# Optimization experiments

Hardware: AMD Instinct MI355X
Metric: run time of the kernel (lower is better)

## Reference

```python
import jax, jax.numpy as jnp
import numpy as np

BATCH, T, N = 8, 2048, 512


def setup_inputs() -> dict:
    key = jax.random.key(0)
    ks = jax.random.split(key, 8)
    scale = 1.0 / np.sqrt(2.0 * (N + N) / 2.0) / np.sqrt(2.0)  # GlorotNormal / sqrt(2)
    u = jax.random.normal(ks[0], (BATCH, T, N), dtype=jnp.float32)
    C_re = jax.random.normal(ks[1], (N, N), dtype=jnp.float32) * scale
    C_im = jax.random.normal(ks[2], (N, N), dtype=jnp.float32) * scale
    B_re = jax.random.normal(ks[3], (N, N), dtype=jnp.float32) * scale
    B_im = jax.random.normal(ks[4], (N, N), dtype=jnp.float32) * scale
    D = jax.random.normal(ks[5], (N,), dtype=jnp.float32)
    # nu drawn from the numerically-stable end of [log(-log rmax), log(-log rmin)]
    nu = jax.random.uniform(ks[6], (N,), minval=-4.6, maxval=-3.7, dtype=jnp.float32)
    theta = jax.random.uniform(ks[7], (N,), minval=0.0, maxval=3.14 / 10, dtype=jnp.float32)
    # gamma initialized as sqrt(1 - |lambda|^2), lambda = exp(-exp(nu) + i*theta)
    gamma = jnp.sqrt(1.0 - jnp.exp(-2.0 * jnp.exp(nu)))
    return {"u": u, "C_re": C_re, "C_im": C_im, "B_re": B_re, "B_im": B_im,
            "D": D, "nu": nu, "theta": theta, "gamma": gamma}


def reference(u, C_re, C_im, B_re, B_im, D, nu, theta, gamma):
    # log_lambda = -exp(nu) + i*theta  (the TF code names this `lambda_`)
    log_lam = (-jnp.exp(nu)).astype(jnp.complex64) + 1j * theta.astype(jnp.complex64)  # (n,)
    t = jnp.arange(u.shape[1], dtype=jnp.float32).astype(jnp.complex64)[:, None]       # (T,1)
    lam_pow = jnp.exp(log_lam[None, :] * t)    # (T,n) == diag(Lambda^t)
    lam_minpow = jnp.exp(-log_lam[None, :] * t)  # (T,n) == diag(Lambda^-t)
    Bm = (B_re + 1j * B_im).astype(jnp.complex64)  # (n,n)
    Cm = (C_re + 1j * C_im).astype(jnp.complex64)  # (n,n)
    # new_u = (gamma * u) @ B   (complex)
    new_u = (gamma * u).astype(jnp.complex64) @ Bm  # (b,t,n)
    # diag einsums in the original are elementwise multiplies
    x = jnp.cumsum(new_u * lam_minpow[None], axis=1) * lam_pow[None]  # (b,t,n)
    y = jnp.real(x @ Cm) + D * u
    return y
```

## Files before the change

### kernel.cpp

```cpp
#include <hip/hip_runtime.h>
#include <hip/hip_bf16.h>
#include <math.h>
#include <stdint.h>

#define BATCH 8
#define T_LEN 2048
#define NDIM 512
#define M_ROWS (BATCH * T_LEN)
#define CHUNK 32
#define NCHUNK (T_LEN / CHUNK)

typedef __attribute__((ext_vector_type(8))) short bf16x8;
typedef __attribute__((ext_vector_type(4))) float floatx4;

__device__ __forceinline__ unsigned short f2bf(float f) {
    union { float f; unsigned u; } v; v.f = f;
    unsigned r = v.u + 0x7fff + ((v.u >> 16) & 1);
    return (unsigned short)(r >> 16);
}
__device__ __forceinline__ float bf2f(unsigned short h) {
    union { unsigned u; float f; } v; v.u = ((unsigned)h) << 16;
    return v.f;
}
__device__ __forceinline__ float bf2f_lo(unsigned u) {
    union { unsigned u; float f; } v; v.u = u << 16; return v.f;
}
__device__ __forceinline__ float bf2f_hi(unsigned u) {
    union { unsigned u; float f; } v; v.u = u & 0xffff0000u; return v.f;
}

__device__ __forceinline__ void gld_lds16(const unsigned short* g, unsigned short* l) {
    __builtin_amdgcn_global_load_lds(
        (const __attribute__((address_space(1))) unsigned int*)(uintptr_t)g,
        (__attribute__((address_space(3))) unsigned int*)(uintptr_t)l,
        16, 0, 0);
}

__global__ __launch_bounds__(256) void k_prep(
    const float* __restrict__ u,
    const float* __restrict__ Bre, const float* __restrict__ Bim,
    const float* __restrict__ Cre, const float* __restrict__ Cim,
    const float* __restrict__ gamma,
    unsigned short* __restrict__ ubf,
    unsigned short* __restrict__ BT, unsigned short* __restrict__ CT)
{
    __shared__ unsigned short tile[32][33];
    const int blk = blockIdx.x;
    if (blk < 4096) {
        size_t i = ((size_t)blk * 256 + threadIdx.x) * 8;
        float4 a = *(const float4*)&u[i];
        float4 b = *(const float4*)&u[i + 4];
        ushort4 p0, p1;
        p0.x = f2bf(a.x); p0.y = f2bf(a.y); p0.z = f2bf(a.z); p0.w = f2bf(a.w);
        p1.x = f2bf(b.x); p1.y = f2bf(b.y); p1.z = f2bf(b.z); p1.w = f2bf(b.w);
        *(ushort4*)&ubf[i] = p0;
        *(ushort4*)&ubf[i + 4] = p1;
        return;
    }
    const int p = blk - 4096;
    const int z = p >> 8;
    const int rem = p & 255;
    const int n0 = (rem & 15) * 32, k0 = (rem >> 4) * 32;
    const float* __restrict__ src = (z == 0) ? Bre : (z == 1) ? Bim : (z == 2) ? Cre : Cim;
    const int tx = threadIdx.x & 31, ty = threadIdx.x >> 5;

#pragma unroll
    for (int j = 0; j < 4; ++j) {
        int k = k0 + ty + j * 8;
        float s = (z < 2) ? gamma[k] : (z == 3 ? -1.f : 1.f);
        tile[ty + j * 8][tx] = f2bf(s * src[(size_t)k * NDIM + n0 + tx]);
    }
    __syncthreads();
#pragma unroll
    for (int j = 0; j < 4; ++j) {
        int n = n0 + ty + j * 8;
        unsigned short v = tile[tx][ty + j * 8];
        if (z == 0)      BT[(size_t)n * 512 + k0 + tx] = v;
        else if (z == 1) BT[(size_t)(512 + n) * 512 + k0 + tx] = v;
        else if (z == 2) CT[(size_t)n * 1024 + k0 + tx] = v;
        else             CT[(size_t)n * 1024 + 512 + k0 + tx] = v;
    }
}

__global__ __launch_bounds__(256) void k_gemm_in(
    const unsigned short* __restrict__ A,
    const unsigned short* __restrict__ BT,
    unsigned short* __restrict__ X)
{
    __shared__ unsigned short As[128 * 32];
    __shared__ unsigned short Bs[128 * 32];
    const int tid = threadIdx.x;
    const int w = tid >> 6, l = tid & 63;
    const int bm = blockIdx.x * 128;
    const int bn = blockIdx.y * 128;
    const int wm = (w & 1) * 64, wn = (w >> 1) * 64;
    const int lm = l & 15, lq = l >> 4;
    const int srow = w * 16 + (l >> 2);
    const int scol = (l & 3) * 8;

    floatx4 acc[4][4];
#pragma unroll
    for (int i = 0; i < 4; ++i)
#pragma unroll
        for (int j = 0; j < 4; ++j) acc[i][j] = (floatx4)0.f;

    for (int k0 = 0; k0 < 512; k0 += 32) {
        gld_lds16(&A[(size_t)(bm + srow) * 512 + k0 + scol],      &As[srow * 32 + scol]);
        gld_lds16(&A[(size_t)(bm + 64 + srow) * 512 + k0 + scol], &As[(64 + srow) * 32 + scol]);
        gld_lds16(&BT[(size_t)(bn + srow) * 512 + k0 + scol],      &Bs[srow * 32 + scol]);
        gld_lds16(&BT[(size_t)(bn + 64 + srow) * 512 + k0 + scol], &Bs[(64 + srow) * 32 + scol]);
        __syncthreads();

        bf16x8 af[4], bfr[4];
#pragma unroll
        for (int i = 0; i < 4; ++i)
            af[i] = *(const bf16x8*)&As[(wm + i * 16 + lm) * 32 + lq * 8];
#pragma unroll
        for (int j = 0; j < 4; ++j)
            bfr[j] = *(const bf16x8*)&Bs[(wn + j * 16 + lm) * 32 + lq * 8];
#pragma unroll
        for (int i = 0; i < 4; ++i)
#pragma unroll
            for (int j = 0; j < 4; ++j)
                acc[i][j] = __builtin_amdgcn_mfma_f32_16x16x32_bf16(af[i], bfr[j], acc[i][j], 0, 0, 0);
        __syncthreads();
    }

#pragma unroll
    for (int i = 0; i < 4; ++i)
#pragma unroll
        for (int j = 0; j < 4; ++j) {
            int col = bn + wn + j * 16 + lm;
#pragma unroll
            for (int r = 0; r < 4; ++r) {
                int row = bm + wm + i * 16 + lq * 4 + r;
                X[(size_t)row * 1024 + col] = f2bf(acc[i][j][r]);
            }
        }
}

__global__ __launch_bounds__(256) void k_scan_carries(
    const unsigned short* __restrict__ X,
    const float* __restrict__ nu, const float* __restrict__ theta,
    float* __restrict__ carry)
{
    const int t2 = threadIdx.x;
    const int n0 = 2 * t2;
    const int b = blockIdx.x >> 6, c = blockIdx.x & 63;
    float r0 = __expf(-__expf(nu[n0]));
    float r1 = __expf(-__expf(nu[n0 + 1]));
    float lre0 = r0 * __cosf(theta[n0]),     lim0 = r0 * __sinf(theta[n0]);
    float lre1 = r1 * __cosf(theta[n0 + 1]), lim1 = r1 * __sinf(theta[n0 + 1]);
    size_t m = (size_t)b * T_LEN + (size_t)c * CHUNK;
    float xre0 = 0.f, xim0 = 0.f, xre1 = 0.f, xim1 = 0.f;
#pragma unroll 8
    for (int t = 0; t < CHUNK; ++t, ++m) {
        unsigned re = *(const unsigned*)&X[m * 1024 + n0];
        unsigned im = *(const unsigned*)&X[m * 1024 + 512 + n0];
        float u0 = bf2f_lo(re), u1 = bf2f_hi(re);
        float v0 = bf2f_lo(im), v1 = bf2f_hi(im);
        float a0 = lre0 * xre0 - lim0 * xim0 + u0;
        float b0 = lre0 * xim0 + lim0 * xre0 + v0;
        float a1 = lre1 * xre1 - lim1 * xim1 + u1;
        float b1 = lre1 * xim1 + lim1 * xre1 + v1;
        xre0 = a0; xim0 = b0; xre1 = a1; xim1 = b1;
    }
    size_t ci = ((size_t)b * NCHUNK + c) * NDIM + n0;
    *(float4*)&carry[ci * 2] = make_float4(xre0, xim0, xre1, xim1);
}

__global__ __launch_bounds__(256) void k_scan_chain(
    const float* __restrict__ carry,
    const float* __restrict__ nu, const float* __restrict__ theta,
    float* __restrict__ pre)
{
    const int tid = blockIdx.x * blockDim.x + threadIdx.x;
    const int b = tid >> 9, n = tid & (NDIM - 1);
    const float ex = __expf(nu[n]);
    const float rC = expf(-ex * (float)CHUNK);
    const float th = theta[n] * (float)CHUNK;
    const float a = rC * cosf(th);
    const float bb = rC * sinf(th);
    float Xre = 0.f, Xim = 0.f;
    for (int c = 0; c < NCHUNK; ++c) {
        size_t idx = ((size_t)b * NCHUNK + c) * NDIM + n;
        *(float2*)&pre[idx * 2] = make_float2(Xre, Xim);
        float2 cv = *(const float2*)&carry[idx * 2];
        float nre = a * Xre - bb * Xim + cv.x;
        float nim = a * Xim + bb * Xre + cv.y;
        Xre = nre; Xim = nim;
    }
}

__global__ __launch_bounds__(256) void k_scan_apply(
    unsigned short* __restrict__ X,
    const float* __restrict__ nu, const float* __restrict__ theta,
    const float* __restrict__ pre)
{
    const int t2 = threadIdx.x;
    const int n0 = 2 * t2;
    const int b = blockIdx.x >> 6, c = blockIdx.x & 63;
    size_t pi = ((size_t)b * NCHUNK + c) * NDIM + n0;
    float4 P = *(const float4*)&pre[pi * 2];
    float r0 = __expf(-__expf(nu[n0]));
    float r1 = __expf(-__expf(nu[n0 + 1]));
    float lre0 = r0 * __cosf(theta[n0]),     lim0 = r0 * __sinf(theta[n0]);
    float lre1 = r1 * __cosf(theta[n0 + 1]), lim1 = r1 * __sinf(theta[n0 + 1]);
    float xre0 = P.x, xim0 = P.y, xre1 = P.z, xim1 = P.w;
    size_t m = (size_t)b * T_LEN + (size_t)c * CHUNK;
#pragma unroll 8
    for (int t = 0; t < CHUNK; ++t, ++m) {
        unsigned re = *(const unsigned*)&X[m * 1024 + n0];
        unsigned im = *(const unsigned*)&X[m * 1024 + 512 + n0];
        float u0 = bf2f_lo(re), u1 = bf2f_hi(re);
        float v0 = bf2f_lo(im), v1 = bf2f_hi(im);
        float a0 = lre0 * xre0 - lim0 * xim0 + u0;
        float b0 = lre0 * xim0 + lim0 * xre0 + v0;
        float a1 = lre1 * xre1 - lim1 * xim1 + u1;
        float b1 = lre1 * xim1 + lim1 * xre1 + v1;
        xre0 = a0; xim0 = b0; xre1 = a1; xim1 = b1;
        unsigned pr = (unsigned)f2bf(xre0) | ((unsigned)f2bf(xre1) << 16);
        unsigned pim = (unsigned)f2bf(xim0) | ((unsigned)f2bf(xim1) << 16);
        *(unsigned*)&X[m * 1024 + n0] = pr;
        *(unsigned*)&X[m * 1024 + 512 + n0] = pim;
    }
}

__global__ __launch_bounds__(256) void k_gemm_out(
    const unsigned short* __restrict__ Xbf,
    const unsigned short* __restrict__ CT,
    const float* __restrict__ D,
    const unsigned short* __restrict__ Ubf,
    float* __restrict__ Y)
{
    __shared__ unsigned short As[128 * 32];
    __shared__ unsigned short Bs[128 * 32];
    const int tid = threadIdx.x;
    const int w = tid >> 6, l = tid & 63;
    const int bm = blockIdx.x * 128;
    const int bn = blockIdx.y * 128;
    const int wm = (w & 1) * 64, wn = (w >> 1) * 64;
    const int lm = l & 15, lq = l >> 4;
    const int srow = w * 16 + (l >> 2);
    const int scol = (l & 3) * 8;

    floatx4 acc[4][4];
#pragma unroll
    for (int i = 0; i < 4; ++i)
#pragma unroll
        for (int j = 0; j < 4; ++j) acc[i][j] = (floatx4)0.f;

    for (int k0 = 0; k0 < 1024; k0 += 32) {
        gld_lds16(&Xbf[(size_t)(bm + srow) * 1024 + k0 + scol],      &As[srow * 32 + scol]);
        gld_lds16(&Xbf[(size_t)(bm + 64 + srow) * 1024 + k0 + scol], &As[(64 + srow) * 32 + scol]);
        gld_lds16(&CT[(size_t)(bn + srow) * 1024 + k0 + scol],       &Bs[srow * 32 + scol]);
        gld_lds16(&CT[(size_t)(bn + 64 + srow) * 1024 + k0 + scol],  &Bs[(64 + srow) * 32 + scol]);
        __syncthreads();

        bf16x8 af[4], bfr[4];
#pragma unroll
        for (int i = 0; i < 4; ++i)
            af[i] = *(const bf16x8*)&As[(wm + i * 16 + lm) * 32 + lq * 8];
#pragma unroll
        for (int j = 0; j < 4; ++j)
            bfr[j] = *(const bf16x8*)&Bs[(wn + j * 16 + lm) * 32 + lq * 8];
#pragma unroll
        for (int i = 0; i < 4; ++i)
#pragma unroll
            for (int j = 0; j < 4; ++j)
                acc[i][j] = __builtin_amdgcn_mfma_f32_16x16x32_bf16(af[i], bfr[j], acc[i][j], 0, 0, 0);
        __syncthreads();
    }

#pragma unroll
    for (int i = 0; i < 4; ++i)
#pragma unroll
        for (int j = 0; j < 4; ++j) {
            int col = bn + wn + j * 16 + lm;
            float dv = D[col];
#pragma unroll
            for (int r = 0; r < 4; ++r) {
                int row = bm + wm + i * 16 + lq * 4 + r;
                size_t off = (size_t)row * NDIM + col;
                Y[off] = acc[i][j][r] + dv * bf2f(Ubf[off]);
            }
        }
}

extern "C" void kernel_launch(void* const* d_in, const int* in_sizes, int n_in,
                              void* d_out, int out_size, void* d_ws, size_t ws_size,
                              hipStream_t stream)
{
    const float* u     = (const float*)d_in[0];
    const float* C_re  = (const float*)d_in[1];
    const float* C_im  = (const float*)d_in[2];
    const float* B_re  = (const float*)d_in[3];
    const float* B_im  = (const float*)d_in[4];
    const float* D     = (const float*)d_in[5];
    const float* nu    = (const float*)d_in[6];
    const float* theta = (const float*)d_in[7];
    const float* gamma = (const float*)d_in[8];
    float* y = (float*)d_out;

    unsigned short* X   = (unsigned short*)d_ws;
    unsigned short* ubf = X + (size_t)M_ROWS * 1024;
    unsigned short* BT  = ubf + (size_t)M_ROWS * 512;
    unsigned short* CT  = BT + (size_t)1024 * 512;
    float* carry = (float*)(CT + (size_t)512 * 1024);
    float* pre   = carry + (size_t)BATCH * NCHUNK * NDIM * 2;

    k_prep<<<4096 + 1024, 256, 0, stream>>>(u, B_re, B_im, C_re, C_im, gamma, ubf, BT, CT);
    k_gemm_in<<<dim3(M_ROWS / 128, 8), 256, 0, stream>>>(ubf, BT, X);
    k_scan_carries<<<BATCH * NCHUNK, 256, 0, stream>>>(X, nu, theta, carry);
    k_scan_chain<<<(BATCH * NDIM) / 256, 256, 0, stream>>>(carry, nu, theta, pre);
    k_scan_apply<<<BATCH * NCHUNK, 256, 0, stream>>>(X, nu, theta, pre);
    k_gemm_out<<<dim3(M_ROWS / 128, 4), 256, 0, stream>>>(X, CT, D, ubf, y);
}
```

Measured before the change: 175.5 us.

## Fuse chunk-carry scan into input GEMM epilogue and drop chain kernel

Weight columns are interleaved so each 128-wide GEMM output tile holds matching real and imaginary halves for 64 channels. The input GEMM then computes per-chunk carries in its epilogue, rereading its own freshly written tile instead of running a separate carry pass over X. The chain kernel is removed: each apply block redoes the carry recurrence over all preceding chunks itself. This saves two launches and one full pass over X, at the cost of quadratic redundant carry work and uncoalesced 2-byte reads in the epilogue.

New measurement: 183.5 us. 4.6% more time.

```diff
diff --git a/kernel.cpp b/kernel.cpp
--- a/kernel.cpp
+++ b/kernel.cpp
@@ -9,6 +9,7 @@
 #define M_ROWS (BATCH * T_LEN)
 #define CHUNK 32
 #define NCHUNK (T_LEN / CHUNK)
+
 
 typedef __attribute__((ext_vector_type(8))) short bf16x8;
 typedef __attribute__((ext_vector_type(4))) float floatx4;
@@ -75,17 +76,30 @@
     for (int j = 0; j < 4; ++j) {
         int n = n0 + ty + j * 8;
         unsigned short v = tile[tx][ty + j * 8];
-        if (z == 0)      BT[(size_t)n * 512 + k0 + tx] = v;
-        else if (z == 1) BT[(size_t)(512 + n) * 512 + k0 + tx] = v;
-        else if (z == 2) CT[(size_t)n * 1024 + k0 + tx] = v;
-        else             CT[(size_t)n * 1024 + 512 + k0 + tx] = v;
+        if (z == 0) {
+            int row = ((n >> 6) << 7) + (n & 63);
+            BT[(size_t)row * 512 + k0 + tx] = v;
+        } else if (z == 1) {
+            int row = ((n >> 6) << 7) + 64 + (n & 63);
+            BT[(size_t)row * 512 + k0 + tx] = v;
+        } else if (z == 2) {
+            int k = k0 + tx;
+            int col = ((k >> 6) << 7) + (k & 63);
+            CT[(size_t)n * 1024 + col] = v;
+        } else {
+            int k = k0 + tx;
+            int col = ((k >> 6) << 7) + 64 + (k & 63);
+            CT[(size_t)n * 1024 + col] = v;
+        }
     }
 }
 
 __global__ __launch_bounds__(256) void k_gemm_in(
     const unsigned short* __restrict__ A,
     const unsigned short* __restrict__ BT,
-    unsigned short* __restrict__ X)
+    const float* __restrict__ nu, const float* __restrict__ theta,
+    unsigned short* __restrict__ X,
+    float* __restrict__ carry)
 {
     __shared__ unsigned short As[128 * 32];
     __shared__ unsigned short Bs[128 * 32];
@@ -137,81 +151,66 @@
                 X[(size_t)row * 1024 + col] = f2bf(acc[i][j][r]);
             }
         }
-}
-
-__global__ __launch_bounds__(256) void k_scan_carries(
-    const unsigned short* __restrict__ X,
+
+    __syncthreads();
+    {
+        const int chunk = tid >> 6;
+        const int ch = tid & 63;
+        const int n = (bn >> 1) + ch;
+        const float rr = __expf(-__expf(nu[n]));
+        const float lre = rr * __cosf(theta[n]);
+        const float lim = rr * __sinf(theta[n]);
+        const unsigned short* pr = &X[(size_t)(bm + chunk * 32) * 1024 + bn + ch];
+        float xre = 0.f, xim = 0.f;
+#pragma unroll 8
+        for (int t = 0; t < 32; ++t) {
+            float ure = bf2f(pr[(size_t)t * 1024]);
+            float uim = bf2f(pr[(size_t)t * 1024 + 64]);
+            float a = lre * xre - lim * xim + ure;
+            float b = lre * xim + lim * xre + uim;
+            xre = a; xim = b;
+        }
+        const int bb = bm >> 11;
+        const int cg = ((bm & 2047) >> 5) + chunk;
+        size_t ci = ((size_t)bb * NCHUNK + cg) * NDIM + n;
+        *(float2*)&carry[ci * 2] = make_float2(xre, xim);
+    }
+}
+
+__global__ __launch_bounds__(256) void k_scan_apply(
+    unsigned short* __restrict__ X,
     const float* __restrict__ nu, const float* __restrict__ theta,
-    float* __restrict__ carry)
+    const float* __restrict__ carry)
 {
     const int t2 = threadIdx.x;
     const int n0 = 2 * t2;
     const int b = blockIdx.x >> 6, c = blockIdx.x & 63;
-    float r0 = __expf(-__expf(nu[n0]));
-    float r1 = __expf(-__expf(nu[n0 + 1]));
-    float lre0 = r0 * __cosf(theta[n0]),     lim0 = r0 * __sinf(theta[n0]);
-    float lre1 = r1 * __cosf(theta[n0 + 1]), lim1 = r1 * __sinf(theta[n0 + 1]);
-    size_t m = (size_t)b * T_LEN + (size_t)c * CHUNK;
+    const float ex0 = __expf(nu[n0]), ex1 = __expf(nu[n0 + 1]);
+    const float r0 = __expf(-ex0), r1 = __expf(-ex1);
+    const float lre0 = r0 * __cosf(theta[n0]),     lim0 = r0 * __sinf(theta[n0]);
+    const float lre1 = r1 * __cosf(theta[n0 + 1]), lim1 = r1 * __sinf(theta[n0 + 1]);
+    const float rc0 = expf(-ex0 * (float)CHUNK), rc1 = expf(-ex1 * (float)CHUNK);
+    const float th0 = theta[n0] * (float)CHUNK,  th1 = theta[n0 + 1] * (float)CHUNK;
+    const float A0 = rc0 * cosf(th0), B0 = rc0 * sinf(th0);
+    const float A1 = rc1 * cosf(th1), B1 = rc1 * sinf(th1);
+
     float xre0 = 0.f, xim0 = 0.f, xre1 = 0.f, xim1 = 0.f;
-#pragma unroll 8
-    for (int t = 0; t < CHUNK; ++t, ++m) {
-        unsigned re = *(const unsigned*)&X[m * 1024 + n0];
-        unsigned im = *(const unsigned*)&X[m * 1024 + 512 + n0];
-        float u0 = bf2f_lo(re), u1 = bf2f_hi(re);
-        float v0 = bf2f_lo(im), v1 = bf2f_hi(im);
-        float a0 = lre0 * xre0 - lim0 * xim0 + u0;
-        float b0 = lre0 * xim0 + lim0 * xre0 + v0;
-        float a1 = lre1 * xre1 - lim1 * xim1 + u1;
-        float b1 = lre1 * xim1 + lim1 * xre1 + v1;
+    for (int cc = 0; cc < c; ++cc) {
+        size_t idx = ((size_t)b * NCHUNK + cc) * NDIM + n0;
+        float4 cv = *(const float4*)&carry[idx * 2];
+        float a0 = A0 * xre0 - B0 * xim0 + cv.x;
+        float b0 = A0 * xim0 + B0 * xre0 + cv.y;
+        float a1 = A1 * xre1 - B1 * xim1 + cv.z;
+        float b1 = A1 * xim1 + B1 * xre1 + cv.w;
         xre0 = a0; xim0 = b0; xre1 = a1; xim1 = b1;
     }
-    size_t ci = ((size_t)b * NCHUNK + c) * NDIM + n0;
-    *(float4*)&carry[ci * 2] = make_float4(xre0, xim0, xre1, xim1);
-}
-
-__global__ __launch_bounds__(256) void k_scan_chain(
-    const float* __restrict__ carry,
-    const float* __restrict__ nu, const float* __restrict__ theta,
-    float* __restrict__ pre)
-{
-    const int tid = blockIdx.x * blockDim.x + threadIdx.x;
-    const int b = tid >> 9, n = tid & (NDIM - 1);
-    const float ex = __expf(nu[n]);
-    const float rC = expf(-ex * (float)CHUNK);
-    const float th = theta[n] * (float)CHUNK;
-    const float a = rC * cosf(th);
-    const float bb = rC * sinf(th);
-    float Xre = 0.f, Xim = 0.f;
-    for (int c = 0; c < NCHUNK; ++c) {
-        size_t idx = ((size_t)b * NCHUNK + c) * NDIM + n;
-        *(float2*)&pre[idx * 2] = make_float2(Xre, Xim);
-        float2 cv = *(const float2*)&carry[idx * 2];
-        float nre = a * Xre - bb * Xim + cv.x;
-        float nim = a * Xim + bb * Xre + cv.y;
-        Xre = nre; Xim = nim;
-    }
-}
-
-__global__ __launch_bounds__(256) void k_scan_apply(
-    unsigned short* __restrict__ X,
-    const float* __restrict__ nu, const float* __restrict__ theta,
-    const float* __restrict__ pre)
-{
-    const int t2 = threadIdx.x;
-    const int n0 = 2 * t2;
-    const int b = blockIdx.x >> 6, c = blockIdx.x & 63;
-    size_t pi = ((size_t)b * NCHUNK + c) * NDIM + n0;
-    float4 P = *(const float4*)&pre[pi * 2];
-    float r0 = __expf(-__expf(nu[n0]));
-    float r1 = __expf(-__expf(nu[n0 + 1]));
-    float lre0 = r0 * __cosf(theta[n0]),     lim0 = r0 * __sinf(theta[n0]);
-    float lre1 = r1 * __cosf(theta[n0 + 1]), lim1 = r1 * __sinf(theta[n0 + 1]);
-    float xre0 = P.x, xim0 = P.y, xre1 = P.z, xim1 = P.w;
+
+    const int recol = ((n0 >> 6) << 7) + (n0 & 63);
     size_t m = (size_t)b * T_LEN + (size_t)c * CHUNK;
 #pragma unroll 8
     for (int t = 0; t < CHUNK; ++t, ++m) {
-        unsigned re = *(const unsigned*)&X[m * 1024 + n0];
-        unsigned im = *(const unsigned*)&X[m * 1024 + 512 + n0];
+        unsigned re = *(const unsigned*)&X[m * 1024 + recol];
+        unsigned im = *(const unsigned*)&X[m * 1024 + recol + 64];
         float u0 = bf2f_lo(re), u1 = bf2f_hi(re);
         float v0 = bf2f_lo(im), v1 = bf2f_hi(im);
         float a0 = lre0 * xre0 - lim0 * xim0 + u0;
@@ -221,8 +220,8 @@
         xre0 = a0; xim0 = b0; xre1 = a1; xim1 = b1;
         unsigned pr = (unsigned)f2bf(xre0) | ((unsigned)f2bf(xre1) << 16);
         unsigned pim = (unsigned)f2bf(xim0) | ((unsigned)f2bf(xim1) << 16);
-        *(unsigned*)&X[m * 1024 + n0] = pr;
-        *(unsigned*)&X[m * 1024 + 512 + n0] = pim;
+        *(unsigned*)&X[m * 1024 + recol] = pr;
+        *(unsigned*)&X[m * 1024 + recol + 64] = pim;
     }
 }
 
@@ -307,12 +306,9 @@
     unsigned short* BT  = ubf + (size_t)M_ROWS * 512;
     unsigned short* CT  = BT + (size_t)1024 * 512;
     float* carry = (float*)(CT + (size_t)512 * 1024);
-    float* pre   = carry + (size_t)BATCH * NCHUNK * NDIM * 2;
 
     k_prep<<<4096 + 1024, 256, 0, stream>>>(u, B_re, B_im, C_re, C_im, gamma, ubf, BT, CT);
-    k_gemm_in<<<dim3(M_ROWS / 128, 8), 256, 0, stream>>>(ubf, BT, X);
-    k_scan_carries<<<BATCH * NCHUNK, 256, 0, stream>>>(X, nu, theta, carry);
-    k_scan_chain<<<(BATCH * NDIM) / 256, 256, 0, stream>>>(carry, nu, theta, pre);
-    k_scan_apply<<<BATCH * NCHUNK, 256, 0, stream>>>(X, nu, theta, pre);
+    k_gemm_in<<<dim3(M_ROWS / 128, 8), 256, 0, stream>>>(ubf, BT, nu, theta, X, carry);
+    k_scan_apply<<<BATCH * NCHUNK, 256, 0, stream>>>(X, nu, theta, carry);
     k_gemm_out<<<dim3(M_ROWS / 128, 4), 256, 0, stream>>>(X, CT, D, ubf, y);
 }
```
